# Performance work log

Hardware: AMD Instinct MI355X
Metric: run time of the kernel (lower is better)

Reference implementation:

```python
import jax, jax.numpy as jnp
import numpy as np

B, T, C, H = 4, 2048, 1024, 16
HD = C // H  # head dim = 64


def setup_inputs() -> dict:
    key = jax.random.key(0)
    k1, k2, k3 = jax.random.split(key, 3)
    scale_in = 1.0 / np.sqrt(C)
    return {
        "x": jax.random.normal(k1, (B, T, C), dtype=jnp.float32),
        "W_attn": jax.random.normal(k2, (C, 3 * C), dtype=jnp.float32) * scale_in,
        "b_attn": jnp.zeros((3 * C,), dtype=jnp.float32),
        "W_proj": jax.random.normal(k3, (C, C), dtype=jnp.float32) * scale_in,
        "b_proj": jnp.zeros((C,), dtype=jnp.float32),
    }


def reference(x, W_attn, b_attn, W_proj, b_proj):
    Bx, Tx, Cx = x.shape
    qkv = x @ W_attn + b_attn                      # [B,T,3C]
    q, k, v = jnp.split(qkv, 3, axis=-1)           # each [B,T,C]
    # [B,T,C] -> [B,H,T,HD]
    q = q.reshape(Bx, Tx, H, HD).transpose(0, 2, 1, 3)
    k = k.reshape(Bx, Tx, H, HD).transpose(0, 2, 1, 3)
    v = v.reshape(Bx, Tx, H, HD).transpose(0, 2, 1, 3)
    att = jnp.einsum("bhqd,bhkd->bhqk", q, k) * (1.0 / np.sqrt(HD))
    causal = jnp.tril(jnp.ones((Tx, Tx), dtype=bool))  # [T,T]
    att = jnp.where(causal[None, None, :, :], att, jnp.float32(-jnp.inf))
    att = jax.nn.softmax(att, axis=-1)
    y = jnp.einsum("bhqk,bhkd->bhqd", att, v)      # [B,H,T,HD]
    y = y.transpose(0, 2, 1, 3).reshape(Bx, Tx, Cx)
    return y @ W_proj + b_proj
```

## Files before the change

kernel.cpp:

```cpp
#include <hip/hip_runtime.h>

typedef _Float16 f16;
typedef __attribute__((ext_vector_type(8))) _Float16 h8;
typedef __attribute__((ext_vector_type(4))) _Float16 h4;
typedef __attribute__((ext_vector_type(8))) short s8;
typedef __attribute__((ext_vector_type(4))) unsigned short u16x4;
typedef __attribute__((ext_vector_type(4))) float f4;
typedef __attribute__((ext_vector_type(16))) float f16x;
typedef __attribute__((ext_vector_type(4))) unsigned u4;

#define MFMA(a, b, c) __builtin_amdgcn_mfma_f32_16x16x32_f16(a, b, c, 0, 0, 0)
#define MFMA32(a, b, c) __builtin_amdgcn_mfma_f32_32x32x16_f16(a, b, c, 0, 0, 0)
#define MFMA32B(a, b, c) __builtin_amdgcn_mfma_f32_32x32x16_bf16(a, b, c, 0, 0, 0)

#define QSCALE 0.18033688011112042f

#define ASM_VMCNT(N) asm volatile("s_waitcnt vmcnt(" #N ")" ::: "memory")

__device__ __forceinline__ void gload16(const void* g, void* l) {
    __builtin_amdgcn_global_load_lds((const __attribute__((address_space(1))) void*)g,
                                     (__attribute__((address_space(3))) void*)l, 16, 0, 0);
}

__device__ __forceinline__ float fexp2(float x) {
    float r;
    asm("v_exp_f32 %0, %1" : "=v"(r) : "v"(x));
    return r;
}

__device__ __forceinline__ unsigned pkb(float a, float b) {
    unsigned r;
    asm("v_cvt_pk_bf16_f32 %0, %1, %2" : "=v"(r) : "v"(a), "v"(b));
    return r;
}

__device__ __forceinline__ unsigned short bf16rn(float x) {
    unsigned u = __builtin_bit_cast(unsigned, x);
    u += 0x7fffu + ((u >> 16) & 1u);
    return (unsigned short)(u >> 16);
}

__device__ __forceinline__ void plswap(unsigned& a, unsigned& b) {
    asm volatile("v_permlane32_swap_b32 %0, %1" : "+v"(a), "+v"(b));
}


__global__ __launch_bounds__(256) void cvt_f16_kernel(const float* __restrict__ in,
                                                      f16* __restrict__ out, int n8) {
    int i = blockIdx.x * blockDim.x + threadIdx.x;
    if (i >= n8) return;
    const float4* p = (const float4*)in + (size_t)i * 2;
    float4 a = p[0], b = p[1];
    h8 o;
    o[0] = (f16)a.x; o[1] = (f16)a.y; o[2] = (f16)a.z; o[3] = (f16)a.w;
    o[4] = (f16)b.x; o[5] = (f16)b.y; o[6] = (f16)b.z; o[7] = (f16)b.w;
    *((h8*)out + i) = o;
}

__global__ __launch_bounds__(256) void transpose_cvt(const float* __restrict__ in,
                                                     f16* __restrict__ out, int R, int Cc) {
    __shared__ float tile[32][33];
    int tx = threadIdx.x, ty = threadIdx.y;
    int c0 = blockIdx.x * 32, r0 = blockIdx.y * 32;
#pragma unroll
    for (int k = 0; k < 32; k += 8)
        tile[ty + k][tx] = in[(size_t)(r0 + ty + k) * Cc + c0 + tx];
    __syncthreads();
#pragma unroll
    for (int k = 0; k < 32; k += 8)
        out[(size_t)(c0 + ty + k) * R + r0 + tx] = (f16)tile[tx][ty + k];
}


__device__ __forceinline__ void gemm_stage_half(const f16* __restrict__ M, int K, int r0, int k0,
                                                f16* dst, int tid, int wave) {
#pragma unroll
    for (int i = 0; i < 2; i++) {
        int s = i * 512 + tid;
        int row = s >> 3;
        int gc = ((s & 7) ^ (row & 7)) * 8;
        gload16(M + (size_t)(r0 + row) * K + k0 + gc, dst + (i * 512 + wave * 64) * 8);
    }
}

__device__ __forceinline__ void gemm_step(const f16* __restrict__ A, const f16* __restrict__ Bt,
                                          int K, int m0, int n0, int t, int nt,
                                          const f16* cA, const f16* cB, f16* nA, f16* nB,
                                          int tid, int lane, int wave, int wm, int wn,
                                          f4 acc[2][4]) {
    ASM_VMCNT(0);
    asm volatile("s_waitcnt lgkmcnt(0)" ::: "memory");
    __builtin_amdgcn_sched_barrier(0);
    __builtin_amdgcn_s_barrier();
    __builtin_amdgcn_sched_barrier(0);
    const bool stage = (t + 1 < nt);
#pragma unroll
    for (int kk = 0; kk < 2; kk++) {
        h8 af[2], bg[4];
#pragma unroll
        for (int im = 0; im < 2; im++) {
            int row = wm + im * 16 + (lane & 15);
            int pc = (kk * 4 + (lane >> 4)) ^ (row & 7);
            af[im] = *(const h8*)(cA + row * 64 + pc * 8);
        }
#pragma unroll
        for (int in = 0; in < 4; in++) {
            int row = wn + in * 16 + (lane & 15);
            int pc = (kk * 4 + (lane >> 4)) ^ (row & 7);
            bg[in] = *(const h8*)(cB + row * 64 + pc * 8);
        }
        if (stage) {
            if (kk == 0) gemm_stage_half(A, K, m0, (t + 1) * 64, nA, tid, wave);
            else         gemm_stage_half(Bt, K, n0, (t + 1) * 64, nB, tid, wave);
        }
        __builtin_amdgcn_s_setprio(1);
#pragma unroll
        for (int im = 0; im < 2; im++)
#pragma unroll
            for (int in = 0; in < 4; in++)
                acc[im][in] = MFMA(af[im], bg[in], acc[im][in]);
        __builtin_amdgcn_s_setprio(0);
    }
}

__device__ __forceinline__ void gemm_core(const f16* __restrict__ A, const f16* __restrict__ Bt,
                                          int K, int m0, int n0,
                                          f16* lA0, f16* lB0, f16* lA1, f16* lB1,
                                          f4 acc[2][4]) {
    const int tid = threadIdx.x, lane = tid & 63, wave = tid >> 6;
    const int wm = (wave >> 1) * 32, wn = (wave & 1) * 64;
    const int nt = K >> 6;

    gemm_stage_half(A, K, m0, 0, lA0, tid, wave);
    gemm_stage_half(Bt, K, n0, 0, lB0, tid, wave);

    for (int t = 0; t < nt; t += 2) {
        gemm_step(A, Bt, K, m0, n0, t, nt, lA0, lB0, lA1, lB1, tid, lane, wave, wm, wn, acc);
        gemm_step(A, Bt, K, m0, n0, t + 1, nt, lA1, lB1, lA0, lB0, tid, lane, wave, wm, wn, acc);
    }
}


__global__ __launch_bounds__(512) void qkv_gemm(const f16* __restrict__ A, const f16* __restrict__ Bt,
                                                const float* __restrict__ bias,
                                                f16* __restrict__ Qo, f16* __restrict__ Ko,
                                                unsigned short* __restrict__ Vo) {
    __shared__ f16 lA[2][128 * 64], lB[2][128 * 64];
    f4 acc[2][4];
    const f4 zz = {0.f, 0.f, 0.f, 0.f};
#pragma unroll
    for (int i = 0; i < 2; i++)
#pragma unroll
        for (int j = 0; j < 4; j++) acc[i][j] = zz;

    const int swz = (blockIdx.x & 7) * 192 + (blockIdx.x >> 3);
    const int nb = swz % 24, mb = swz / 24;
    gemm_core(A, Bt, 1024, mb * 128, nb * 128, lA[0], lB[0], lA[1], lB[1], acc);

    const int lane = threadIdx.x & 63, wave = threadIdx.x >> 6;
    const int wm = (wave >> 1) * 32, wn = (wave & 1) * 64;
#pragma unroll
    for (int im = 0; im < 2; im++) {
        int m4 = mb * 128 + wm + im * 16 + (lane >> 4) * 4;
        int b = m4 >> 11, t0 = m4 & 2047;
#pragma unroll
        for (int in = 0; in < 4; in++) {
            int n = nb * 128 + wn + in * 16 + (lane & 15);
            float bb = bias[n];
            int sec = n >> 10, cc = n & 1023, hh = cc >> 6, d = cc & 63;
            if (sec == 2) {
                u16x4 pv;
#pragma unroll
                for (int r = 0; r < 4; r++) pv[r] = bf16rn(acc[im][in][r] + bb);
                *(u16x4*)(Vo + (size_t)(b * 16 + hh) * 131072 + (t0 >> 5) * 2048 + d * 32 +
                          (t0 & 31)) = pv;
            } else {
                f16* dst = sec ? Ko : Qo;
                float sc = sec ? 1.0f : QSCALE;
                size_t base = ((size_t)(b * 16 + hh) * 2048 + t0) * 64 + d;
#pragma unroll
                for (int r = 0; r < 4; r++)
                    dst[base + (size_t)r * 64] = (f16)((acc[im][in][r] + bb) * sc);
            }
        }
    }
}


__global__ __launch_bounds__(512) void proj_gemm(const f16* __restrict__ A, const f16* __restrict__ Bt,
                                                 const float* __restrict__ bias,
                                                 float* __restrict__ out) {
    __shared__ f16 lA[2][128 * 64], lB[2][128 * 64];
    f4 acc[2][4];
    const f4 zz = {0.f, 0.f, 0.f, 0.f};
#pragma unroll
    for (int i = 0; i < 2; i++)
#pragma unroll
        for (int j = 0; j < 4; j++) acc[i][j] = zz;

    const int swz = (blockIdx.x & 7) * 64 + (blockIdx.x >> 3);
    const int nb = swz & 7, mb = swz >> 3;
    gemm_core(A, Bt, 1024, mb * 128, nb * 128, lA[0], lB[0], lA[1], lB[1], acc);

    const int lane = threadIdx.x & 63, wave = threadIdx.x >> 6;
    const int wm = (wave >> 1) * 32, wn = (wave & 1) * 64;
#pragma unroll
    for (int im = 0; im < 2; im++) {
        int m4 = mb * 128 + wm + im * 16 + (lane >> 4) * 4;
#pragma unroll
        for (int in = 0; in < 4; in++) {
            int n = nb * 128 + wn + in * 16 + (lane & 15);
            float bb = bias[n];
#pragma unroll
            for (int r = 0; r < 4; r++)
                out[(size_t)(m4 + r) * 1024 + n] = acc[im][in][r] + bb;
        }
    }
}


__device__ __forceinline__ void attn_tile(int k0, bool last, bool stage_next,
                                          int lane, int hi, int ln,
                                          const f16* __restrict__ Kb,
                                          const unsigned short* __restrict__ Vb,
                                          const f16* lKcur, f16* lKnxt,
                                          const h8 (&qf)[4], s8 (&vf)[2][2], s8 (&vfn)[2][2],
                                          float& lpart, f16x& y0, f16x& y1) {
    if (stage_next) {
#pragma unroll
        for (int i = 0; i < 4; i++) {
            int s = i * 64 + lane;
            int row = s >> 3;
            int gc = ((s & 7) ^ (row & 7)) * 8;
            gload16(Kb + (size_t)(k0 + 32 + row) * 64 + gc, lKnxt + i * 512);
        }
#pragma unroll
        for (int ks = 0; ks < 2; ks++)
#pragma unroll
            for (int j = 0; j < 2; j++)
                vfn[ks][j] = *(const s8*)(Vb + (size_t)((k0 >> 5) + 1) * 2048 +
                                          (j * 32 + ln) * 32 + ks * 16 + hi * 8);
        ASM_VMCNT(8);
    } else {
        ASM_VMCNT(0);
    }
    __builtin_amdgcn_sched_barrier(0);

    f16x s0;
#pragma unroll
    for (int r = 0; r < 16; r++) s0[r] = 0.f;
    __builtin_amdgcn_s_setprio(1);
#pragma unroll
    for (int dd = 0; dd < 4; dd++) {
        const int c = (dd * 2 + hi) ^ (ln & 7);
        h8 ka = *(const h8*)(lKcur + ln * 64 + c * 8);
        s0 = MFMA32(ka, qf[dd], s0);
    }
    __builtin_amdgcn_s_setprio(0);

    if (last) {
#pragma unroll
        for (int r = 0; r < 16; r++) {
            int kl = (r & 3) + 8 * (r >> 2) + 4 * hi;
            if (kl > ln) s0[r] = -3e38f;
        }
    }

    float ls = 0.f;
#pragma unroll
    for (int r = 0; r < 16; r++) {
        float p = fexp2(s0[r]);
        s0[r] = p;
        ls += p;
    }
    lpart += ls;

    s8 pa[2];
    {
        unsigned a0 = pkb(s0[0], s0[1]), a1 = pkb(s0[2], s0[3]);
        unsigned b0 = pkb(s0[4], s0[5]), b1 = pkb(s0[6], s0[7]);
        plswap(a0, b0); plswap(a1, b1);
        u4 w0; w0[0] = a0; w0[1] = a1; w0[2] = b0; w0[3] = b1;
        pa[0] = __builtin_bit_cast(s8, w0);
        unsigned c0 = pkb(s0[8], s0[9]), c1 = pkb(s0[10], s0[11]);
        unsigned d0 = pkb(s0[12], s0[13]), d1 = pkb(s0[14], s0[15]);
        plswap(c0, d0); plswap(c1, d1);
        u4 w1; w1[0] = c0; w1[1] = c1; w1[2] = d0; w1[3] = d1;
        pa[1] = __builtin_bit_cast(s8, w1);
    }

    __builtin_amdgcn_s_setprio(1);
#pragma unroll
    for (int ks = 0; ks < 2; ks++) {
        y0 = MFMA32B(pa[ks], vf[ks][0], y0);
        y1 = MFMA32B(pa[ks], vf[ks][1], y1);
    }
    __builtin_amdgcn_s_setprio(0);
}

__global__ __launch_bounds__(64) void attn_kernel(const f16* __restrict__ Q,
                                                  const f16* __restrict__ K,
                                                  const unsigned short* __restrict__ Vg,
                                                  f16* __restrict__ O) {
    __shared__ f16 lK[2][2048];
    const int lane = threadIdx.x;
    const int hi = lane >> 5, ln = lane & 31;
    const int bh = blockIdx.x & 63;
    const int p = (int)(blockIdx.x >> 6);
    const f16* Qb = Q + (size_t)bh * 2048 * 64;
    const f16* Kb = K + (size_t)bh * 2048 * 64;
    const unsigned short* Vb = Vg + (size_t)bh * 131072;
    const int b = bh >> 4, hh = bh & 15;

    for (int ph = 0; ph < 2; ph++) {
        const int qt = ph ? p : 63 - p;
        const int qw = qt * 32;

        h8 qf[4];
#pragma unroll
        for (int dd = 0; dd < 4; dd++)
            qf[dd] = *(const h8*)(Qb + (size_t)(qw + ln) * 64 + dd * 16 + hi * 8);

        float lpart = 0.f;
        f16x y0, y1;
#pragma unroll
        for (int r = 0; r < 16; r++) { y0[r] = 0.f; y1[r] = 0.f; }

        const int nt = qt + 1;

        s8 vfA[2][2], vfB[2][2];
#pragma unroll
        for (int i = 0; i < 4; i++) {
            int s = i * 64 + lane;
            int row = s >> 3;
            int gc = ((s & 7) ^ (row & 7)) * 8;
            gload16(Kb + (size_t)row * 64 + gc, &lK[0][i * 512]);
        }
#pragma unroll
        for (int ks = 0; ks < 2; ks++)
#pragma unroll
            for (int j = 0; j < 2; j++)
                vfA[ks][j] = *(const s8*)(Vb + (size_t)(j * 32 + ln) * 32 + ks * 16 + hi * 8);

        for (int it = 0; it < nt; it += 2) {
            attn_tile(it * 32, it == nt - 1, it + 1 < nt, lane, hi, ln, Kb, Vb,
                      &lK[0][0], &lK[1][0], qf, vfA, vfB, lpart, y0, y1);
            if (it + 1 < nt)
                attn_tile((it + 1) * 32, it + 1 == nt - 1, it + 2 < nt, lane, hi, ln, Kb, Vb,
                          &lK[1][0], &lK[0][0], qf, vfB, vfA, lpart, y0, y1);
        }

        float lT = lpart + __shfl_xor(lpart, 32);
        float inv = 1.0f / lT;
#pragma unroll
        for (int r = 0; r < 16; r++) {
            int crow = (r & 3) + 8 * (r >> 2) + 4 * hi;
            float invr = __shfl(inv, crow);
            size_t base = ((size_t)(b * 2048 + qw + crow)) * 1024 + hh * 64 + ln;
            O[base] = (f16)(y0[r] * invr);
            O[base + 32] = (f16)(y1[r] * invr);
        }
    }
}


extern "C" void kernel_launch(void* const* d_in, const int* in_sizes, int n_in,
                              void* d_out, int out_size, void* d_ws, size_t ws_size,
                              hipStream_t stream) {
    const float* x      = (const float*)d_in[0];
    const float* W_attn = (const float*)d_in[1];
    const float* b_attn = (const float*)d_in[2];
    const float* W_proj = (const float*)d_in[3];
    const float* b_proj = (const float*)d_in[4];
    float* out = (float*)d_out;

    char* ws = (char*)d_ws;
    f16* xb  = (f16*)ws;
    f16* Wat = (f16*)(ws + 16777216);
    f16* Wpt = (f16*)(ws + 16777216 + 6291456);
    unsigned short* Vt = (unsigned short*)(ws + 16777216 + 6291456 + 2097152);
    f16* Qs  = (f16*)d_out;
    f16* Ks  = (f16*)((char*)d_out + 16777216);

    cvt_f16_kernel<<<4096, 256, 0, stream>>>(x, xb, 1048576);
    transpose_cvt<<<dim3(96, 32), dim3(32, 8), 0, stream>>>(W_attn, Wat, 1024, 3072);
    transpose_cvt<<<dim3(32, 32), dim3(32, 8), 0, stream>>>(W_proj, Wpt, 1024, 1024);
    qkv_gemm<<<1536, 512, 0, stream>>>(xb, Wat, b_attn, Qs, Ks, Vt);
    attn_kernel<<<2048, 64, 0, stream>>>(Qs, Ks, Vt, xb);
    proj_gemm<<<512, 512, 0, stream>>>(xb, Wpt, b_proj, out);
}
```

Baseline: 173.0 us.

## Deepen GEMM global-to-LDS pipeline from two to four stages

The QKV and projection GEMMs now rotate through four LDS buffers instead of two and prefetch three k-tiles ahead. The vmcnt waits are relaxed so only the oldest tile's loads must land before each step. The goal is to hide more global load latency behind MFMA work. In exchange, LDS use per block doubles to 128 KB, which can limit occupancy to one block per CU, and the waitcnt accounting adds fragile bookkeeping.

```diff
diff --git a/kernel.cpp b/kernel.cpp
--- a/kernel.cpp
+++ b/kernel.cpp
@@ -88,12 +88,14 @@
                                           const f16* cA, const f16* cB, f16* nA, f16* nB,
                                           int tid, int lane, int wave, int wm, int wn,
                                           f4 acc[2][4]) {
-    ASM_VMCNT(0);
+    if (t + 2 < nt) { ASM_VMCNT(8); }
+    else if (t + 1 < nt) { ASM_VMCNT(4); }
+    else { ASM_VMCNT(0); }
     asm volatile("s_waitcnt lgkmcnt(0)" ::: "memory");
     __builtin_amdgcn_sched_barrier(0);
     __builtin_amdgcn_s_barrier();
     __builtin_amdgcn_sched_barrier(0);
-    const bool stage = (t + 1 < nt);
+    const bool stage = (t + 3 < nt);
 #pragma unroll
     for (int kk = 0; kk < 2; kk++) {
         h8 af[2], bg[4];
@@ -110,8 +112,8 @@
             bg[in] = *(const h8*)(cB + row * 64 + pc * 8);
         }
         if (stage) {
-            if (kk == 0) gemm_stage_half(A, K, m0, (t + 1) * 64, nA, tid, wave);
-            else         gemm_stage_half(Bt, K, n0, (t + 1) * 64, nB, tid, wave);
+            if (kk == 0) gemm_stage_half(A, K, m0, (t + 3) * 64, nA, tid, wave);
+            else         gemm_stage_half(Bt, K, n0, (t + 3) * 64, nB, tid, wave);
         }
         __builtin_amdgcn_s_setprio(1);
 #pragma unroll
@@ -124,19 +126,28 @@
 }
 
 __device__ __forceinline__ void gemm_core(const f16* __restrict__ A, const f16* __restrict__ Bt,
-                                          int K, int m0, int n0,
-                                          f16* lA0, f16* lB0, f16* lA1, f16* lB1,
+                                          int K, int m0, int n0, f16* lds,
                                           f4 acc[2][4]) {
     const int tid = threadIdx.x, lane = tid & 63, wave = tid >> 6;
     const int wm = (wave >> 1) * 32, wn = (wave & 1) * 64;
     const int nt = K >> 6;
-
-    gemm_stage_half(A, K, m0, 0, lA0, tid, wave);
-    gemm_stage_half(Bt, K, n0, 0, lB0, tid, wave);
-
-    for (int t = 0; t < nt; t += 2) {
-        gemm_step(A, Bt, K, m0, n0, t, nt, lA0, lB0, lA1, lB1, tid, lane, wave, wm, wn, acc);
-        gemm_step(A, Bt, K, m0, n0, t + 1, nt, lA1, lB1, lA0, lB0, tid, lane, wave, wm, wn, acc);
+    f16* a0 = lds;              f16* b0 = lds + 4 * 8192;
+    f16* a1 = lds + 1 * 8192;   f16* b1 = lds + 5 * 8192;
+    f16* a2 = lds + 2 * 8192;   f16* b2 = lds + 6 * 8192;
+    f16* a3 = lds + 3 * 8192;   f16* b3 = lds + 7 * 8192;
+
+    gemm_stage_half(A, K, m0, 0, a0, tid, wave);
+    gemm_stage_half(Bt, K, n0, 0, b0, tid, wave);
+    gemm_stage_half(A, K, m0, 64, a1, tid, wave);
+    gemm_stage_half(Bt, K, n0, 64, b1, tid, wave);
+    gemm_stage_half(A, K, m0, 128, a2, tid, wave);
+    gemm_stage_half(Bt, K, n0, 128, b2, tid, wave);
+
+    for (int t = 0; t < nt; t += 4) {
+        gemm_step(A, Bt, K, m0, n0, t,     nt, a0, b0, a3, b3, tid, lane, wave, wm, wn, acc);
+        gemm_step(A, Bt, K, m0, n0, t + 1, nt, a1, b1, a0, b0, tid, lane, wave, wm, wn, acc);
+        gemm_step(A, Bt, K, m0, n0, t + 2, nt, a2, b2, a1, b1, tid, lane, wave, wm, wn, acc);
+        gemm_step(A, Bt, K, m0, n0, t + 3, nt, a3, b3, a2, b2, tid, lane, wave, wm, wn, acc);
     }
 }
 
@@ -145,7 +156,7 @@
                                                 const float* __restrict__ bias,
                                                 f16* __restrict__ Qo, f16* __restrict__ Ko,
                                                 unsigned short* __restrict__ Vo) {
-    __shared__ f16 lA[2][128 * 64], lB[2][128 * 64];
+    __shared__ f16 lds[8 * 8192];
     f4 acc[2][4];
     const f4 zz = {0.f, 0.f, 0.f, 0.f};
 #pragma unroll
@@ -155,7 +166,7 @@
 
     const int swz = (blockIdx.x & 7) * 192 + (blockIdx.x >> 3);
     const int nb = swz % 24, mb = swz / 24;
-    gemm_core(A, Bt, 1024, mb * 128, nb * 128, lA[0], lB[0], lA[1], lB[1], acc);
+    gemm_core(A, Bt, 1024, mb * 128, nb * 128, lds, acc);
 
     const int lane = threadIdx.x & 63, wave = threadIdx.x >> 6;
     const int wm = (wave >> 1) * 32, wn = (wave & 1) * 64;
@@ -190,7 +201,7 @@
 __global__ __launch_bounds__(512) void proj_gemm(const f16* __restrict__ A, const f16* __restrict__ Bt,
                                                  const float* __restrict__ bias,
                                                  float* __restrict__ out) {
-    __shared__ f16 lA[2][128 * 64], lB[2][128 * 64];
+    __shared__ f16 lds[8 * 8192];
     f4 acc[2][4];
     const f4 zz = {0.f, 0.f, 0.f, 0.f};
 #pragma unroll
@@ -200,7 +211,7 @@
 
     const int swz = (blockIdx.x & 7) * 64 + (blockIdx.x >> 3);
     const int nb = swz & 7, mb = swz >> 3;
-    gemm_core(A, Bt, 1024, mb * 128, nb * 128, lA[0], lB[0], lA[1], lB[1], acc);
+    gemm_core(A, Bt, 1024, mb * 128, nb * 128, lds, acc);
 
     const int lane = threadIdx.x & 63, wave = threadIdx.x >> 6;
     const int wm = (wave >> 1) * 32, wn = (wave & 1) * 64;
```

New measurement: 191.9 us. 1.11x slower.
